# Kernel tuning notes

Measured on AMD Instinct MI355X. Metric: run time of the kernel, lower is better.

The kernel has to match this reference:

```python
import jax, jax.numpy as jnp
import numpy as np

N_NODES = 50000
N_EDGES = 800000
IN_CH = 128
OUT_CH = 128
TIME_DIM = 64


def setup_inputs() -> dict:
    key = jax.random.key(0)
    ks = jax.random.split(key, 7)
    x = jax.random.normal(ks[0], (N_NODES, IN_CH), dtype=jnp.float32)
    edge_index = jax.random.randint(ks[1], (2, N_EDGES), 0, N_NODES, dtype=jnp.int64)
    edge_t = jax.random.uniform(ks[2], (N_EDGES,), dtype=jnp.float32)
    # parameters
    freqs = jax.random.normal(ks[3], (TIME_DIM // 2,), dtype=jnp.float32)
    fan = IN_CH + TIME_DIM
    lim = float(np.sqrt(1.0 / fan))
    lin_w = jax.random.uniform(ks[4], (OUT_CH, fan), minval=-lim, maxval=lim, dtype=jnp.float32)
    lin_b = jax.random.uniform(ks[5], (OUT_CH,), minval=-lim, maxval=lim, dtype=jnp.float32)
    glim = float(np.sqrt(6.0 / (1 + OUT_CH)))
    attn = jax.random.uniform(ks[6], (1, OUT_CH), minval=-glim, maxval=glim, dtype=jnp.float32)
    return {"x": x, "edge_index": edge_index, "edge_t": edge_t,
            "freqs": freqs, "lin_w": lin_w, "lin_b": lin_b, "attn": attn}


def reference(x, edge_index, edge_t, freqs, lin_w, lin_b, attn):
    src, dst = edge_index[0], edge_index[1]
    n_nodes = x.shape[0]
    # time encoding: [E, time_dim]
    ang = edge_t[:, None] * freqs * (2.0 * jnp.pi)
    edge_attr = jnp.concatenate([jnp.sin(ang), jnp.cos(ang)], axis=-1)
    # gather source features and project: h = tanh(Linear(cat(x_j, te)))
    msg = jnp.concatenate([x[src], edge_attr], axis=-1)        # [E, in+time]
    h = jnp.tanh(msg @ lin_w.T + lin_b)                        # [E, out]
    # segment softmax over destination nodes
    alpha = (h * attn).sum(axis=-1)                            # [E]
    seg_max = jax.ops.segment_max(alpha, dst, num_segments=n_nodes)
    ex = jnp.exp(alpha - seg_max[dst])
    denom = jax.ops.segment_sum(ex, dst, num_segments=n_nodes)
    w = ex / (denom[dst] + 1e-16)
    # scatter-add aggregation
    out = jax.ops.segment_sum(h * w[:, None], dst, num_segments=n_nodes)
    return out
```

## Files before the change

kernel.cpp:

```cpp
#include <hip/hip_runtime.h>
#include <hip/hip_bf16.h>
#include <math.h>

#define IN_CHN 128
#define OUT_CHN 128
#define KD 192
#define TM 64

typedef __bf16 bf16x8 __attribute__((ext_vector_type(8)));
typedef float f32x4 __attribute__((ext_vector_type(4)));

static __device__ __forceinline__ unsigned short f2b(float f) {
    return __builtin_bit_cast(unsigned short, (__bf16)f);
}
static __device__ __forceinline__ float b2f(unsigned short b) {
    return __uint_as_float(((unsigned int)b) << 16);
}
static __device__ __forceinline__ float fast_tanh(float x) {
    float e = __expf(2.0f * x);
    return 1.0f - 2.0f * __builtin_amdgcn_rcpf(e + 1.0f);
}

#define GLL16(gsrc, ldst) \
    __builtin_amdgcn_global_load_lds( \
        (const __attribute__((address_space(1))) unsigned int*)(gsrc), \
        (__attribute__((address_space(3))) unsigned int*)(ldst), 16, 0, 0)

#define LDS_BARRIER() do { \
    asm volatile("s_waitcnt lgkmcnt(0)" ::: "memory"); \
    __builtin_amdgcn_s_barrier(); \
    __builtin_amdgcn_sched_barrier(0); \
} while (0)


__global__ __launch_bounds__(256) void cvt_x(const float* __restrict__ x,
    unsigned short* __restrict__ xb, long long n8)
{
    long long i = (long long)blockIdx.x * 256 + threadIdx.x;
    if (i >= n8) return;
    const float4* src = (const float4*)(x + i * 8);
    float4 v0 = src[0], v1 = src[1];
    ushort4 p0 = { f2b(v0.x), f2b(v0.y), f2b(v0.z), f2b(v0.w) };
    ushort4 p1 = { f2b(v1.x), f2b(v1.y), f2b(v1.z), f2b(v1.w) };
    *(ushort4*)(xb + i * 8)     = p0;
    *(ushort4*)(xb + i * 8 + 4) = p1;
}


__global__ __launch_bounds__(256) void count_deg(const int* __restrict__ ei,
                                                 int* __restrict__ deg, int E) {
    int e = blockIdx.x * 256 + threadIdx.x;
    if (e < E) atomicAdd(&deg[ei[E + e]], 1);
}

static __device__ __forceinline__ int wave_incl_scan(int v, int lane) {
    #pragma unroll
    for (int off = 1; off < 64; off <<= 1) {
        int t = __shfl_up(v, off);
        if (lane >= off) v += t;
    }
    return v;
}

__global__ __launch_bounds__(256) void scan_local(const int* __restrict__ deg,
    int* __restrict__ offs, int* __restrict__ partial, int Nn)
{
    __shared__ int wsum[4];
    int tid = threadIdx.x, lane = tid & 63, wid = tid >> 6;
    int i = blockIdx.x * 256 + tid;
    int v = (i < Nn) ? deg[i] : 0;
    int incl = wave_incl_scan(v, lane);
    if (lane == 63) wsum[wid] = incl;
    __syncthreads();
    int wpre = 0;
    for (int w = 0; w < wid; ++w) wpre += wsum[w];
    if (i < Nn) offs[i] = wpre + incl - v;
    if (tid == 255) partial[blockIdx.x] = wpre + incl;
}

__global__ __launch_bounds__(256) void scan_partial(int* __restrict__ partial, int nparts)
{
    __shared__ int wsum[4];
    int tid = threadIdx.x, lane = tid & 63, wid = tid >> 6;
    int v = (tid < nparts) ? partial[tid] : 0;
    int incl = wave_incl_scan(v, lane);
    if (lane == 63) wsum[wid] = incl;
    __syncthreads();
    int wpre = 0;
    for (int w = 0; w < wid; ++w) wpre += wsum[w];
    if (tid < nparts) partial[tid] = wpre + incl - v;
}

__global__ __launch_bounds__(256) void finalize_offs(int* __restrict__ offs,
    const int* __restrict__ partial, int* __restrict__ cursor, int Nn, int E)
{
    int i = blockIdx.x * 256 + threadIdx.x;
    if (i < Nn) {
        int o = offs[i] + partial[i >> 8];
        offs[i] = o; cursor[i] = o;
        if (i == Nn - 1) offs[Nn] = E;
    }
}

__global__ __launch_bounds__(256) void fill_perm(const int* __restrict__ ei,
    const float* __restrict__ et, int* __restrict__ cursor,
    uint2* __restrict__ mt, int* __restrict__ nid, int E)
{
    int e = blockIdx.x * 256 + threadIdx.x;
    if (e < E) {
        int d = ei[E + e];
        int pos = atomicAdd(&cursor[d], 1);
        mt[pos] = make_uint2((unsigned)ei[e], __float_as_uint(et[e]));
        nid[pos] = d;
    }
}


__device__ __forceinline__ void load_meta(const uint2* __restrict__ mt,
    int tile, int E, int rbase, int g, int trow, int sv[2], float& tsv)
{
    int e0 = tile * TM;
    #pragma unroll
    for (int i = 0; i < 2; ++i) {
        int e = e0 + rbase + i * 4 + g;
        sv[i] = (int)mt[e < E ? e : E - 1].x;
    }
    int el = e0 + trow;
    tsv = __uint_as_float(mt[el < E ? el : E - 1].y);
}

__global__ __launch_bounds__(512) void gemm_fused(
    const unsigned short* __restrict__ xb, const uint2* __restrict__ mt,
    const int* __restrict__ nid, const int* __restrict__ offs,
    const float* __restrict__ freqs, const float* __restrict__ lw,
    const float* __restrict__ lb, const float* __restrict__ attn,
    float* __restrict__ out, float* __restrict__ den_g,
    int E, int Nn, int n_tiles, int kq, int kr)
{
    __shared__ unsigned short xs[2][TM][128];
    __shared__ unsigned short te[TM * 64];
    __shared__ unsigned short hx[TM][136];
    __shared__ float exs[TM];

    const int b    = blockIdx.x;
    const int t0   = b * kq + min(b, kr);
    const int cnt  = kq + (b < kr ? 1 : 0);
    if (cnt <= 0 || t0 >= n_tiles) return;
    const int tend = min(t0 + cnt, n_tiles);
    const int be0  = t0 * TM;
    const int bend = min(tend * TM, E);

    const int tid  = threadIdx.x;
    const int lane = tid & 63;
    const int wv   = tid >> 6;
    const int c16  = lane & 15;
    const int g    = lane >> 4;
    const int wbase = wv * 16;
    const int rbase = wv * 8;
    const int trow  = tid >> 3;
    const int tpart = tid & 7;
    const int sub  = lane >> 4;
    const int chl  = lane & 15;

    bf16x8 Wf[6];
    #pragma unroll
    for (int kk = 0; kk < 6; ++kk) {
        const float* wp = lw + (size_t)(wbase + c16) * KD + kk * 32 + g * 8;
        float4 v0 = *(const float4*)wp;
        float4 v1 = *(const float4*)(wp + 4);
        bf16x8 bb;
        bb[0] = (__bf16)v0.x; bb[1] = (__bf16)v0.y; bb[2] = (__bf16)v0.z; bb[3] = (__bf16)v0.w;
        bb[4] = (__bf16)v1.x; bb[5] = (__bf16)v1.y; bb[6] = (__bf16)v1.z; bb[7] = (__bf16)v1.w;
        Wf[kk] = bb;
    }
    const f32x4 bias_v = *(const f32x4*)(lb   + wbase + g * 4);
    const f32x4 attn_v = *(const f32x4*)(attn + wbase + g * 4);

    const float coff = (tpart >= 4) ? 1.5707963267948966f : 0.0f;
    float frv[8];
    #pragma unroll
    for (int j = 0; j < 8; ++j) frv[j] = freqs[(tpart & 3) * 8 + j] * 6.283185307179586f;

    int n0 = nid[be0];
    int cur_node = n0 + ((wv - (n0 & 7)) & 7);
    float a[8];
    #pragma unroll
    for (int q = 0; q < 8; ++q) a[q] = 0.0f;
    float den = 0.0f;

    float ts_cur, ts_nxt;
    int sv_nxt[2];
    {
        int sv0[2];
        load_meta(mt, t0, E, rbase, g, trow, sv0, ts_cur);
        #pragma unroll
        for (int i = 0; i < 2; ++i) {
            const int rlo = (rbase + i * 4 + g) & 15;
            const unsigned short* gsrc = xb + (size_t)sv0[i] * IN_CHN + ((c16 ^ rlo) * 8);
            GLL16(gsrc, &xs[0][rbase + i * 4][0]);
        }
        int t1 = t0 + 1;
        load_meta(mt, t1 < tend ? t1 : tend - 1, E, rbase, g, trow, sv_nxt, ts_nxt);
    }

    int cur = 0;
    for (int tile = t0; tile < tend; ++tile) {
        const int e0 = tile * TM;
        const int e1 = e0 + TM;

        ushort4 tp[2];
        {
            float v[8];
            #pragma unroll
            for (int j = 0; j < 8; ++j)
                v[j] = __sinf(ts_cur * frv[j] + coff);
            tp[0] = (ushort4){ f2b(v[0]), f2b(v[1]), f2b(v[2]), f2b(v[3]) };
            tp[1] = (ushort4){ f2b(v[4]), f2b(v[5]), f2b(v[6]), f2b(v[7]) };
        }
        int sv2[2]; float ts2;
        {
            int t2 = tile + 2;
            load_meta(mt, t2 < tend ? t2 : tend - 1, E, rbase, g, trow, sv2, ts2);
        }

        __syncthreads();

        if (tile + 1 < tend) {
            #pragma unroll
            for (int i = 0; i < 2; ++i) {
                const int rlo = (rbase + i * 4 + g) & 15;
                const unsigned short* gsrc = xb + (size_t)sv_nxt[i] * IN_CHN + ((c16 ^ rlo) * 8);
                GLL16(gsrc, &xs[cur ^ 1][rbase + i * 4][0]);
            }
        }
        {
            unsigned short* tr = &te[trow * 64];
            int slot = (tpart ^ (trow & 7)) * 8;
            *(ushort4*)(tr + slot)     = tp[0];
            *(ushort4*)(tr + slot + 4) = tp[1];
            if (tid < TM) exs[tid] = 0.0f;
        }

        LDS_BARRIER();

        f32x4 acc[4];
        #pragma unroll
        for (int mi = 0; mi < 4; ++mi) acc[mi] = (f32x4){0.f, 0.f, 0.f, 0.f};

        __builtin_amdgcn_s_setprio(1);
        const unsigned short* xsc = &xs[cur][0][0];
        #pragma unroll
        for (int mi = 0; mi < 4; ++mi) {
            const int r = mi * 16 + c16;
            const unsigned short* xrow = xsc + r * 128;
            #pragma unroll
            for (int kk = 0; kk < 4; ++kk) {
                const int slot = ((kk << 2) + g) ^ c16;
                bf16x8 av = __builtin_bit_cast(bf16x8, *(const uint4*)(xrow + slot * 8));
                acc[mi] = __builtin_amdgcn_mfma_f32_16x16x32_bf16(Wf[kk], av, acc[mi], 0, 0, 0);
            }
            const unsigned short* trw = &te[r * 64];
            bf16x8 s8 = __builtin_bit_cast(bf16x8, *(const uint4*)(trw + ((g ^ (r & 7)) * 8)));
            bf16x8 c8 = __builtin_bit_cast(bf16x8, *(const uint4*)(trw + (((g + 4) ^ (r & 7)) * 8)));
            acc[mi] = __builtin_amdgcn_mfma_f32_16x16x32_bf16(Wf[4], s8, acc[mi], 0, 0, 0);
            acc[mi] = __builtin_amdgcn_mfma_f32_16x16x32_bf16(Wf[5], c8, acc[mi], 0, 0, 0);
        }
        __builtin_amdgcn_s_setprio(0);

        #pragma unroll
        for (int mi = 0; mi < 4; ++mi) {
            const int r = mi * 16 + c16;
            f32x4 z = acc[mi];
            float p = 0.0f;
            #pragma unroll
            for (int q = 0; q < 4; ++q) {
                float h = fast_tanh(z[q] + bias_v[q]);
                z[q] = h;
                p = fmaf(h, attn_v[q], p);
            }
            ushort4 pv = (ushort4){ f2b(z[0]), f2b(z[1]), f2b(z[2]), f2b(z[3]) };
            *(ushort4*)&hx[r][wbase + g * 4] = pv;
            p += __shfl_xor(p, 16);
            p += __shfl_xor(p, 32);
            if (g == 0) atomicAdd(&exs[r], p);
        }

        LDS_BARRIER();

        while (cur_node < Nn) {
            int s  = offs[cur_node];
            if (s >= e1) break;
            int en = offs[cur_node + 1];
            int lo = s > e0 ? s : e0;
            int hi = en < e1 ? en : e1;
            for (int i = lo + sub; i < hi; i += 4) {
                int li = i - e0;
                float ex = __expf(exs[li]);
                uint4 hv = *(const uint4*)&hx[li][chl * 8];
                den += ex;
                unsigned int hw[4] = { hv.x, hv.y, hv.z, hv.w };
                #pragma unroll
                for (int q = 0; q < 4; ++q) {
                    a[2*q]   = fmaf(ex, b2f((unsigned short)(hw[q] & 0xFFFFu)), a[2*q]);
                    a[2*q+1] = fmaf(ex, b2f((unsigned short)(hw[q] >> 16)),     a[2*q+1]);
                }
            }
            if (en <= e1) {
                #pragma unroll
                for (int q = 0; q < 8; ++q) {
                    a[q] += __shfl_xor(a[q], 16);
                    a[q] += __shfl_xor(a[q], 32);
                }
                float ds = den + __shfl_xor(den, 16);
                ds += __shfl_xor(ds, 32);
                float* op = out + (size_t)cur_node * OUT_CHN + chl * 8;
                if (s >= be0) {
                    if (sub == 0) {
                        *(float4*)op       = (float4){a[0], a[1], a[2], a[3]};
                        *(float4*)(op + 4) = (float4){a[4], a[5], a[6], a[7]};
                        if (chl == 0) den_g[cur_node] = ds;
                    }
                } else {
                    if (sub == 0) {
                        #pragma unroll
                        for (int q = 0; q < 8; ++q) atomicAdd(op + q, a[q]);
                        if (chl == 0) atomicAdd(&den_g[cur_node], ds);
                    }
                }
                #pragma unroll
                for (int q = 0; q < 8; ++q) a[q] = 0.0f;
                den = 0.0f;
                cur_node += 8;
            } else break;
        }

        ts_cur = ts_nxt; ts_nxt = ts2;
        sv_nxt[0] = sv2[0]; sv_nxt[1] = sv2[1];
        cur ^= 1;
    }

    if (cur_node < Nn) {
        int s = offs[cur_node];
        if (s < bend && offs[cur_node + 1] > bend) {
            #pragma unroll
            for (int q = 0; q < 8; ++q) {
                a[q] += __shfl_xor(a[q], 16);
                a[q] += __shfl_xor(a[q], 32);
            }
            float ds = den + __shfl_xor(den, 16);
            ds += __shfl_xor(ds, 32);
            if (sub == 0) {
                float* op = out + (size_t)cur_node * OUT_CHN + chl * 8;
                #pragma unroll
                for (int q = 0; q < 8; ++q) atomicAdd(op + q, a[q]);
                if (chl == 0) atomicAdd(&den_g[cur_node], ds);
            }
        }
    }
}


__global__ __launch_bounds__(256) void normalize(float* __restrict__ out,
    const float* __restrict__ den_g, int Nn)
{
    int gid = blockIdx.x * 256 + threadIdx.x;
    int n = gid >> 5;
    if (n >= Nn) return;
    int c = (gid & 31) * 4;
    float rs = __builtin_amdgcn_rcpf(den_g[n] + 1e-16f);
    float4* p = (float4*)(out + (size_t)n * OUT_CHN + c);
    float4 v = *p;
    v.x *= rs; v.y *= rs; v.z *= rs; v.w *= rs;
    *p = v;
}


extern "C" void kernel_launch(void* const* d_in, const int* in_sizes, int n_in,
                              void* d_out, int out_size, void* d_ws, size_t ws_size,
                              hipStream_t stream) {
    const float* x     = (const float*)d_in[0];
    const int*   ei    = (const int*)d_in[1];
    const float* et    = (const float*)d_in[2];
    const float* freqs = (const float*)d_in[3];
    const float* lw    = (const float*)d_in[4];
    const float* lb    = (const float*)d_in[5];
    const float* attn  = (const float*)d_in[6];
    float* out = (float*)d_out;

    const int E  = in_sizes[2];
    const int Nn = in_sizes[0] / IN_CHN;

    char* ws = (char*)d_ws;
    uint2* mt      = (uint2*)ws;         size_t off = (size_t)E * sizeof(uint2);
    int*   nid     = (int*)(ws + off);   off += (size_t)E * sizeof(int);
    unsigned short* xb = (unsigned short*)(ws + off); off += (size_t)Nn * IN_CHN * sizeof(unsigned short);
    float* den_g   = (float*)(ws + off); off += (size_t)Nn * sizeof(float);
    int*   deg     = (int*)(ws + off);   off += (size_t)Nn * sizeof(int);
    int*   offs    = (int*)(ws + off);   off += (size_t)(Nn + 1) * sizeof(int);
    int*   cursor  = (int*)(ws + off);   off += (size_t)Nn * sizeof(int);
    int*   partial = (int*)(ws + off);

    const int nblk = (Nn + 255) / 256;
    const int eblk = (E + 255) / 256;

    long long n8 = (long long)Nn * IN_CHN / 8;
    cvt_x<<<(unsigned)((n8 + 255) / 256), 256, 0, stream>>>(x, xb, n8);

    hipMemsetAsync(deg, 0, (size_t)Nn * sizeof(int), stream);
    count_deg<<<eblk, 256, 0, stream>>>(ei, deg, E);
    scan_local<<<nblk, 256, 0, stream>>>(deg, offs, partial, Nn);
    scan_partial<<<1, 256, 0, stream>>>(partial, nblk);
    finalize_offs<<<nblk, 256, 0, stream>>>(offs, partial, cursor, Nn, E);
    fill_perm<<<eblk, 256, 0, stream>>>(ei, et, cursor, mt, nid, E);

    hipMemsetAsync(out, 0, (size_t)out_size * sizeof(float), stream);
    hipMemsetAsync(den_g, 0, (size_t)Nn * sizeof(float), stream);

    const int n_tiles = (E + TM - 1) / TM;
    const int NB = 512;
    const int kq = n_tiles / NB, kr = n_tiles % NB;
    gemm_fused<<<NB, 512, 0, stream>>>(xb, mt, nid, offs, freqs, lw, lb, attn,
                                       out, den_g, E, Nn, n_tiles, kq, kr);

    normalize<<<(Nn * 32 + 255) / 256, 256, 0, stream>>>(out, den_g, Nn);
}
```

Baseline: 259.3 us.

## Drop memsets and nid array, fuse scan kernels, defer boundary atomics to fixup

Several changes land together. Zeroing of deg is folded into the bf16 conversion kernel, and the out/den_g memsets are removed by having blocks write owned nodes directly, with empty nodes zeroed in normalize. The separate partial-scan kernel is merged into finalize, the per-edge nid array is replaced by a binary search over offs, and the te/hx LDS buffers now share one region behind an extra barrier. Boundary nodes spanning blocks go to a side buffer that a new fixup kernel adds with atomics. Block count goes from 512 to 768. The intent is to cut launches, memsets and memory traffic, at the cost of an extra barrier and a small fixup pass.

```diff
diff --git a/kernel.cpp b/kernel.cpp
--- a/kernel.cpp
+++ b/kernel.cpp
@@ -6,6 +6,7 @@
 #define OUT_CHN 128
 #define KD 192
 #define TM 64
+#define HXP 136
 
 typedef __bf16 bf16x8 __attribute__((ext_vector_type(8)));
 typedef float f32x4 __attribute__((ext_vector_type(4)));
@@ -33,17 +34,22 @@
 } while (0)
 
 
-__global__ __launch_bounds__(256) void cvt_x(const float* __restrict__ x,
-    unsigned short* __restrict__ xb, long long n8)
+__global__ __launch_bounds__(256) void cvt_init(const float* __restrict__ x,
+    unsigned short* __restrict__ xb, int* __restrict__ deg,
+    int* __restrict__ side_node, long long n8, int Nn, int nb)
 {
     long long i = (long long)blockIdx.x * 256 + threadIdx.x;
-    if (i >= n8) return;
-    const float4* src = (const float4*)(x + i * 8);
-    float4 v0 = src[0], v1 = src[1];
-    ushort4 p0 = { f2b(v0.x), f2b(v0.y), f2b(v0.z), f2b(v0.w) };
-    ushort4 p1 = { f2b(v1.x), f2b(v1.y), f2b(v1.z), f2b(v1.w) };
-    *(ushort4*)(xb + i * 8)     = p0;
-    *(ushort4*)(xb + i * 8 + 4) = p1;
+    if (i < n8) {
+        const float4* src = (const float4*)(x + i * 8);
+        float4 v0 = src[0], v1 = src[1];
+        ushort4 p0 = { f2b(v0.x), f2b(v0.y), f2b(v0.z), f2b(v0.w) };
+        ushort4 p1 = { f2b(v1.x), f2b(v1.y), f2b(v1.z), f2b(v1.w) };
+        *(ushort4*)(xb + i * 8)     = p0;
+        *(ushort4*)(xb + i * 8 + 4) = p1;
+    }
+    int t = (int)i;
+    if (t < Nn) deg[t] = 0;
+    if (t < nb) side_node[t] = -1;
 }
 
 
@@ -78,25 +84,21 @@
     if (tid == 255) partial[blockIdx.x] = wpre + incl;
 }
 
-__global__ __launch_bounds__(256) void scan_partial(int* __restrict__ partial, int nparts)
+__global__ __launch_bounds__(256) void finalize2(int* __restrict__ offs,
+    const int* __restrict__ partial, int* __restrict__ cursor,
+    int Nn, int E, int nblk)
 {
     __shared__ int wsum[4];
-    int tid = threadIdx.x, lane = tid & 63, wid = tid >> 6;
-    int v = (tid < nparts) ? partial[tid] : 0;
-    int incl = wave_incl_scan(v, lane);
-    if (lane == 63) wsum[wid] = incl;
+    int b = blockIdx.x, tid = threadIdx.x, lane = tid & 63, wid = tid >> 6;
+    int v = (tid < b && tid < nblk) ? partial[tid] : 0;
+    #pragma unroll
+    for (int off = 32; off > 0; off >>= 1) v += __shfl_xor(v, off);
+    if (lane == 0) wsum[wid] = v;
     __syncthreads();
-    int wpre = 0;
-    for (int w = 0; w < wid; ++w) wpre += wsum[w];
-    if (tid < nparts) partial[tid] = wpre + incl - v;
-}
-
-__global__ __launch_bounds__(256) void finalize_offs(int* __restrict__ offs,
-    const int* __restrict__ partial, int* __restrict__ cursor, int Nn, int E)
-{
-    int i = blockIdx.x * 256 + threadIdx.x;
+    int bp = wsum[0] + wsum[1] + wsum[2] + wsum[3];
+    int i = b * 256 + tid;
     if (i < Nn) {
-        int o = offs[i] + partial[i >> 8];
+        int o = offs[i] + bp;
         offs[i] = o; cursor[i] = o;
         if (i == Nn - 1) offs[Nn] = E;
     }
@@ -104,14 +106,13 @@
 
 __global__ __launch_bounds__(256) void fill_perm(const int* __restrict__ ei,
     const float* __restrict__ et, int* __restrict__ cursor,
-    uint2* __restrict__ mt, int* __restrict__ nid, int E)
+    uint2* __restrict__ mt, int E)
 {
     int e = blockIdx.x * 256 + threadIdx.x;
     if (e < E) {
         int d = ei[E + e];
         int pos = atomicAdd(&cursor[d], 1);
         mt[pos] = make_uint2((unsigned)ei[e], __float_as_uint(et[e]));
-        nid[pos] = d;
     }
 }
 
@@ -131,16 +132,19 @@
 
 __global__ __launch_bounds__(512) void gemm_fused(
     const unsigned short* __restrict__ xb, const uint2* __restrict__ mt,
-    const int* __restrict__ nid, const int* __restrict__ offs,
+    const int* __restrict__ offs,
     const float* __restrict__ freqs, const float* __restrict__ lw,
     const float* __restrict__ lb, const float* __restrict__ attn,
     float* __restrict__ out, float* __restrict__ den_g,
+    int* __restrict__ side_node, float* __restrict__ side_den,
+    float* __restrict__ side_val,
     int E, int Nn, int n_tiles, int kq, int kr)
 {
     __shared__ unsigned short xs[2][TM][128];
-    __shared__ unsigned short te[TM * 64];
-    __shared__ unsigned short hx[TM][136];
-    __shared__ float exs[TM];
+    __shared__ __align__(16) unsigned short uni[TM * HXP + 128];
+    unsigned short* te = uni;
+    unsigned short* hx = uni;
+    float* exs = (float*)(uni + TM * HXP);
 
     const int b    = blockIdx.x;
     const int t0   = b * kq + min(b, kr);
@@ -181,7 +185,15 @@
     #pragma unroll
     for (int j = 0; j < 8; ++j) frv[j] = freqs[(tpart & 3) * 8 + j] * 6.283185307179586f;
 
-    int n0 = nid[be0];
+    int n0;
+    {
+        int lo = 0, hi = Nn;
+        while (lo + 1 < hi) {
+            int mid = (lo + hi) >> 1;
+            if (offs[mid] <= be0) lo = mid; else hi = mid;
+        }
+        n0 = lo;
+    }
     int cur_node = n0 + ((wv - (n0 & 7)) & 7);
     float a[8];
     #pragma unroll
@@ -267,6 +279,8 @@
         }
         __builtin_amdgcn_s_setprio(0);
 
+        LDS_BARRIER();
+
         #pragma unroll
         for (int mi = 0; mi < 4; ++mi) {
             const int r = mi * 16 + c16;
@@ -279,7 +293,7 @@
                 p = fmaf(h, attn_v[q], p);
             }
             ushort4 pv = (ushort4){ f2b(z[0]), f2b(z[1]), f2b(z[2]), f2b(z[3]) };
-            *(ushort4*)&hx[r][wbase + g * 4] = pv;
+            *(ushort4*)&hx[r * HXP + wbase + g * 4] = pv;
             p += __shfl_xor(p, 16);
             p += __shfl_xor(p, 32);
             if (g == 0) atomicAdd(&exs[r], p);
@@ -296,7 +310,7 @@
             for (int i = lo + sub; i < hi; i += 4) {
                 int li = i - e0;
                 float ex = __expf(exs[li]);
-                uint4 hv = *(const uint4*)&hx[li][chl * 8];
+                uint4 hv = *(const uint4*)&hx[li * HXP + chl * 8];
                 den += ex;
                 unsigned int hw[4] = { hv.x, hv.y, hv.z, hv.w };
                 #pragma unroll
@@ -313,19 +327,11 @@
                 }
                 float ds = den + __shfl_xor(den, 16);
                 ds += __shfl_xor(ds, 32);
-                float* op = out + (size_t)cur_node * OUT_CHN + chl * 8;
-                if (s >= be0) {
-                    if (sub == 0) {
-                        *(float4*)op       = (float4){a[0], a[1], a[2], a[3]};
-                        *(float4*)(op + 4) = (float4){a[4], a[5], a[6], a[7]};
-                        if (chl == 0) den_g[cur_node] = ds;
-                    }
-                } else {
-                    if (sub == 0) {
-                        #pragma unroll
-                        for (int q = 0; q < 8; ++q) atomicAdd(op + q, a[q]);
-                        if (chl == 0) atomicAdd(&den_g[cur_node], ds);
-                    }
+                if (sub == 0) {
+                    float* op = out + (size_t)cur_node * OUT_CHN + chl * 8;
+                    *(float4*)op       = (float4){a[0], a[1], a[2], a[3]};
+                    *(float4*)(op + 4) = (float4){a[4], a[5], a[6], a[7]};
+                    if (chl == 0) den_g[cur_node] = ds;
                 }
                 #pragma unroll
                 for (int q = 0; q < 8; ++q) a[q] = 0.0f;
@@ -350,25 +356,46 @@
             float ds = den + __shfl_xor(den, 16);
             ds += __shfl_xor(ds, 32);
             if (sub == 0) {
-                float* op = out + (size_t)cur_node * OUT_CHN + chl * 8;
-                #pragma unroll
-                for (int q = 0; q < 8; ++q) atomicAdd(op + q, a[q]);
-                if (chl == 0) atomicAdd(&den_g[cur_node], ds);
-            }
-        }
-    }
+                float* sv = side_val + (size_t)b * OUT_CHN + chl * 8;
+                *(float4*)sv       = (float4){a[0], a[1], a[2], a[3]};
+                *(float4*)(sv + 4) = (float4){a[4], a[5], a[6], a[7]};
+                if (chl == 0) {
+                    side_den[b] = ds;
+                    side_node[b] = cur_node;
+                }
+            }
+        }
+    }
+}
+
+
+__global__ __launch_bounds__(256) void fixup(const int* __restrict__ side_node,
+    const float* __restrict__ side_den, const float* __restrict__ side_val,
+    float* __restrict__ out, float* __restrict__ den_g, int nb)
+{
+    int w = (blockIdx.x * 256 + threadIdx.x) >> 6;
+    int lane = threadIdx.x & 63;
+    if (w >= nb) return;
+    int node = side_node[w];
+    if (node < 0) return;
+    const float* sv = side_val + (size_t)w * OUT_CHN;
+    float* op = out + (size_t)node * OUT_CHN;
+    atomicAdd(op + lane * 2,     sv[lane * 2]);
+    atomicAdd(op + lane * 2 + 1, sv[lane * 2 + 1]);
+    if (lane == 0) atomicAdd(&den_g[node], side_den[w]);
 }
 
 
 __global__ __launch_bounds__(256) void normalize(float* __restrict__ out,
-    const float* __restrict__ den_g, int Nn)
+    const float* __restrict__ den_g, const int* __restrict__ offs, int Nn)
 {
     int gid = blockIdx.x * 256 + threadIdx.x;
     int n = gid >> 5;
     if (n >= Nn) return;
     int c = (gid & 31) * 4;
+    float4* p = (float4*)(out + (size_t)n * OUT_CHN + c);
+    if (offs[n + 1] == offs[n]) { *p = (float4){0, 0, 0, 0}; return; }
     float rs = __builtin_amdgcn_rcpf(den_g[n] + 1e-16f);
-    float4* p = (float4*)(out + (size_t)n * OUT_CHN + c);
     float4 v = *p;
     v.x *= rs; v.y *= rs; v.z *= rs; v.w *= rs;
     *p = v;
@@ -389,38 +416,39 @@
 
     const int E  = in_sizes[2];
     const int Nn = in_sizes[0] / IN_CHN;
+    const int NB = 768;
 
     char* ws = (char*)d_ws;
     uint2* mt      = (uint2*)ws;         size_t off = (size_t)E * sizeof(uint2);
-    int*   nid     = (int*)(ws + off);   off += (size_t)E * sizeof(int);
     unsigned short* xb = (unsigned short*)(ws + off); off += (size_t)Nn * IN_CHN * sizeof(unsigned short);
     float* den_g   = (float*)(ws + off); off += (size_t)Nn * sizeof(float);
     int*   deg     = (int*)(ws + off);   off += (size_t)Nn * sizeof(int);
     int*   offs    = (int*)(ws + off);   off += (size_t)(Nn + 1) * sizeof(int);
     int*   cursor  = (int*)(ws + off);   off += (size_t)Nn * sizeof(int);
-    int*   partial = (int*)(ws + off);
+    int*   partial = (int*)(ws + off);   off += 1024 * sizeof(int);
+    int*   side_node = (int*)(ws + off); off += (size_t)NB * sizeof(int);
+    float* side_den  = (float*)(ws + off); off += (size_t)NB * sizeof(float);
+    float* side_val  = (float*)(ws + off);
 
     const int nblk = (Nn + 255) / 256;
     const int eblk = (E + 255) / 256;
 
     long long n8 = (long long)Nn * IN_CHN / 8;
-    cvt_x<<<(unsigned)((n8 + 255) / 256), 256, 0, stream>>>(x, xb, n8);
-
-    hipMemsetAsync(deg, 0, (size_t)Nn * sizeof(int), stream);
+    cvt_init<<<(unsigned)((n8 + 255) / 256), 256, 0, stream>>>(x, xb, deg, side_node, n8, Nn, NB);
+
     count_deg<<<eblk, 256, 0, stream>>>(ei, deg, E);
     scan_local<<<nblk, 256, 0, stream>>>(deg, offs, partial, Nn);
-    scan_partial<<<1, 256, 0, stream>>>(partial, nblk);
-    finalize_offs<<<nblk, 256, 0, stream>>>(offs, partial, cursor, Nn, E);
-    fill_perm<<<eblk, 256, 0, stream>>>(ei, et, cursor, mt, nid, E);
-
-    hipMemsetAsync(out, 0, (size_t)out_size * sizeof(float), stream);
-    hipMemsetAsync(den_g, 0, (size_t)Nn * sizeof(float), stream);
+    finalize2<<<nblk, 256, 0, stream>>>(offs, partial, cursor, Nn, E, nblk);
+    fill_perm<<<eblk, 256, 0, stream>>>(ei, et, cursor, mt, E);
 
     const int n_tiles = (E + TM - 1) / TM;
-    const int NB = 512;
     const int kq = n_tiles / NB, kr = n_tiles % NB;
-    gemm_fused<<<NB, 512, 0, stream>>>(xb, mt, nid, offs, freqs, lw, lb, attn,
-                                       out, den_g, E, Nn, n_tiles, kq, kr);
-
-    normalize<<<(Nn * 32 + 255) / 256, 256, 0, stream>>>(out, den_g, Nn);
-}
+    gemm_fused<<<NB, 512, 0, stream>>>(xb, mt, offs, freqs, lw, lb, attn,
+                                       out, den_g, side_node, side_den, side_val,
+                                       E, Nn, n_tiles, kq, kr);
+
+    fixup<<<(NB * 64 + 255) / 256, 256, 0, stream>>>(side_node, side_den, side_val,
+                                                     out, den_g, NB);
+
+    normalize<<<(Nn * 32 + 255) / 256, 256, 0, stream>>>(out, den_g, offs, Nn);
+}
```

Result: faster. 250.4 us (-3.4%).
